# Kernel tuning notes

Hardware: AMD Instinct MI355X
Metric: run time of the kernel (lower is better)

## Reference

```python
import jax, jax.numpy as jnp
import numpy as np

N = 100000   # nodes
R = 4        # relation types
E = 200000   # edges per relation
IN, HID, OUT = 128, 256, 256


def _hetero_conv(x, ew, src, dst, W, b):
    """One HeteroGraphConv(mean) layer of GraphConv(norm='both') per relation.
    x: [N, d_in], ew: [R, E, d_in], src/dst: [R, E], W: [R, d_in, d_out], b: [R, d_out]."""
    outs = []
    for r in range(R):  # small fixed relation set
        s, d = src[r], dst[r]
        ones = jnp.ones((E,), x.dtype)
        deg_out = jax.ops.segment_sum(ones, s, num_segments=N)
        deg_in = jax.ops.segment_sum(ones, d, num_segments=N)
        ns = jax.lax.rsqrt(jnp.clip(deg_out, 1.0))  # src-side norm
        nd = jax.lax.rsqrt(jnp.clip(deg_in, 1.0))   # dst-side norm
        # gather src feats, scale, edge-weight, scatter-sum to dst
        m = x[s] * ns[s][:, None] * ew[r]                       # [E, d_in]
        agg = jax.ops.segment_sum(m, d, num_segments=N)          # [N, d_in]
        agg = agg * nd[:, None]
        outs.append(agg @ W[r] + b[r])
    return sum(outs) / R


def setup_inputs() -> dict:
    key = jax.random.key(0)
    ks = jax.random.split(key, 12)
    sc = 0.05
    return {
        "node_feat": jax.random.normal(ks[0], (N, IN), jnp.float32),
        "edge_w_raw": jax.random.normal(ks[1], (R, E, IN), jnp.float32),
        "src": jax.random.randint(ks[2], (R, E), 0, N),
        "dst": jax.random.randint(ks[3], (R, E), 0, N),
        "Wn": jax.random.normal(ks[4], (IN, HID), jnp.float32) * sc,
        "bn": jax.random.normal(ks[5], (HID,), jnp.float32) * sc,
        "Wr": jax.random.normal(ks[6], (IN, HID), jnp.float32) * sc,
        "br": jax.random.normal(ks[7], (HID,), jnp.float32) * sc,
        "W1": jax.random.normal(ks[8], (R, HID, HID), jnp.float32) * sc,
        "b1": jax.random.normal(ks[9], (R, HID), jnp.float32) * sc,
        "W2": jax.random.normal(ks[10], (R, HID, OUT), jnp.float32) * sc,
        "b2": jax.random.normal(ks[11], (R, OUT), jnp.float32) * sc,
    }


def reference(node_feat, edge_w_raw, src, dst, Wn, bn, Wr, br, W1, b1, W2, b2):
    # rela_fc on raw edge weights (shared by both layers)
    ew = jnp.einsum('rei,ih->reh', edge_w_raw, Wr) + br          # [R, E, HID]
    # node_fc
    x0 = node_feat @ Wn + bn                                      # [N, HID]
    h1 = _hetero_conv(x0, ew, src, dst, W1, b1)                   # [N, HID]
    h2 = _hetero_conv(h1, ew, src, dst, W2, b2)                   # [N, OUT]
    return h2
```

## Files before the change

kernel.cpp:

```cpp
#include <hip/hip_runtime.h>

constexpr int Nn  = 100000;
constexpr int Rr  = 4;
constexpr int Ee  = 200000;
constexpr int Din = 128;
constexpr int Dh  = 256;
constexpr int RN  = Rr * Nn;
constexpr int RE  = Rr * Ee;

typedef float  f32x4  __attribute__((ext_vector_type(4)));
typedef __bf16 bf16x4 __attribute__((ext_vector_type(4)));
typedef __bf16 bf16x8 __attribute__((ext_vector_type(8)));

__global__ __launch_bounds__(256) void count_deg_kernel(
    const int* __restrict__ src, const int* __restrict__ dst,
    int* __restrict__ dego, int* __restrict__ degi) {
  int i = blockIdx.x * 256 + threadIdx.x;
  if (i < RE) {
    int r = i / Ee;
    atomicAdd(&dego[r * Nn + src[i]], 1);
    atomicAdd(&degi[r * Nn + dst[i]], 1);
  }
}

__global__ __launch_bounds__(256) void norms_kernel(
    const int* __restrict__ dego, const int* __restrict__ degi,
    float* __restrict__ ns, float* __restrict__ nd) {
  int i = blockIdx.x * 256 + threadIdx.x;
  if (i < RN) {
    int a = dego[i]; if (a < 1) a = 1;
    int b = degi[i]; if (b < 1) b = 1;
    ns[i] = rsqrtf((float)a);
    nd[i] = rsqrtf((float)b);
  }
}

__device__ inline int block_excl_scan_256(int tsum, int tid, int* wsum) {
  int lane = tid & 63, w = tid >> 6;
  int inc = tsum;
#pragma unroll
  for (int off = 1; off < 64; off <<= 1) {
    int t = __shfl_up(inc, off);
    if (lane >= off) inc += t;
  }
  if (lane == 63) wsum[w] = inc;
  __syncthreads();
  int woff = 0;
  for (int i = 0; i < w; ++i) woff += wsum[i];
  return woff + inc - tsum;
}

__global__ __launch_bounds__(256) void scan1_kernel(
    const int* __restrict__ in, int* __restrict__ out,
    int* __restrict__ partials, int n) {
  __shared__ int wsum[4];
  int tid = threadIdx.x;
  int base = blockIdx.x * 1024 + tid * 4;
  int v[4];
#pragma unroll
  for (int j = 0; j < 4; ++j) v[j] = (base + j < n) ? in[base + j] : 0;
  int tsum = v[0] + v[1] + v[2] + v[3];
  int off = block_excl_scan_256(tsum, tid, wsum);
  int run = off;
#pragma unroll
  for (int j = 0; j < 4; ++j) {
    if (base + j < n) out[base + j] = run;
    run += v[j];
  }
  __syncthreads();
  if (tid == 0) partials[blockIdx.x] = wsum[0] + wsum[1] + wsum[2] + wsum[3];
}

__global__ __launch_bounds__(256) void scan2_kernel(int* __restrict__ p, int n) {
  __shared__ int wsum[4];
  int tid = threadIdx.x;
  int e0 = (2 * tid     < n) ? p[2 * tid]     : 0;
  int e1 = (2 * tid + 1 < n) ? p[2 * tid + 1] : 0;
  int off = block_excl_scan_256(e0 + e1, tid, wsum);
  if (2 * tid     < n) p[2 * tid]     = off;
  if (2 * tid + 1 < n) p[2 * tid + 1] = off + e0;
}

__global__ __launch_bounds__(256) void scan3_kernel(
    int* __restrict__ out, const int* __restrict__ partials, int n) {
  int i = blockIdx.x * 256 + threadIdx.x;
  if (i < n) out[i] += partials[i >> 10];
  if (i == 0) out[n] = RE;
}

__global__ __launch_bounds__(256) void fill_eid_kernel(
    const int* __restrict__ dst, int* __restrict__ cursor,
    int* __restrict__ eid) {
  int i = blockIdx.x * 256 + threadIdx.x;
  if (i < RE) {
    int r = i / Ee;
    int pos = atomicAdd(&cursor[r * Nn + dst[i]], 1);
    eid[pos] = i;
  }
}

__global__ __launch_bounds__(256) void bias_combine_kernel(
    const float* __restrict__ b1, const float* __restrict__ b2,
    float* __restrict__ cb) {
  int i = threadIdx.x;
  cb[i]      = 0.25f * (b1[i] + b1[Dh + i] + b1[2 * Dh + i] + b1[3 * Dh + i]);
  cb[Dh + i] = 0.25f * (b2[i] + b2[Dh + i] + b2[2 * Dh + i] + b2[3 * Dh + i]);
}

__global__ __launch_bounds__(256) void transpose_bf16_kernel(
    const float* __restrict__ in, __bf16* __restrict__ outp, int K) {
  __shared__ float t[32][33];
  int kb = blockIdx.x * 32, nb = blockIdx.y * 32;
  int tx = threadIdx.x & 31, ty = threadIdx.x >> 5;
#pragma unroll
  for (int j = 0; j < 32; j += 8)
    t[ty + j][tx] = in[(size_t)(kb + ty + j) * Dh + nb + tx];
  __syncthreads();
#pragma unroll
  for (int j = 0; j < 32; j += 8)
    outp[(size_t)(nb + ty + j) * K + kb + tx] = (__bf16)t[tx][ty + j];
}

template <int K, bool ABF16, bool OUT_BF16>
__global__ __launch_bounds__(256, 2) void gemm_n256(
    const void* __restrict__ Av, const __bf16* __restrict__ Bt,
    void* __restrict__ Cv, const float* __restrict__ bias,
    float alpha, int M) {
  __shared__ __bf16 As[128][40];
  __shared__ __bf16 Bs[256][40];
  const int tid  = threadIdx.x;
  const int m0   = blockIdx.x * 128;
  const int w    = tid >> 6;
  const int lane = tid & 63;
  const int wr = w >> 1, wc = w & 1;
  const int l15 = lane & 15, quad = lane >> 4;
  f32x4 acc[4][8] = {};

  for (int kt = 0; kt < K / 32; ++kt) {
    if constexpr (ABF16) {
      const __bf16* A = (const __bf16*)Av;
#pragma unroll
      for (int it = 0; it < 2; ++it) {
        int i = tid + it * 256;
        int row = i >> 2;
        int col = (i & 3) << 3;
        int grow = m0 + row;
        bf16x8 v;
#pragma unroll
        for (int j = 0; j < 8; ++j) v[j] = (__bf16)0.f;
        if (grow < M)
          v = *(const bf16x8*)(A + (size_t)grow * K + kt * 32 + col);
        *(bf16x8*)&As[row][col] = v;
      }
    } else {
      const float* A = (const float*)Av;
#pragma unroll
      for (int it = 0; it < 4; ++it) {
        int i = tid + it * 256;
        int row = i >> 3;
        int col = (i & 7) << 2;
        int grow = m0 + row;
        f32x4 v = {0.f, 0.f, 0.f, 0.f};
        if (grow < M)
          v = *(const f32x4*)(A + (size_t)grow * K + kt * 32 + col);
        bf16x4 bv;
        bv[0] = (__bf16)v[0]; bv[1] = (__bf16)v[1];
        bv[2] = (__bf16)v[2]; bv[3] = (__bf16)v[3];
        *(bf16x4*)&As[row][col] = bv;
      }
    }
#pragma unroll
    for (int it = 0; it < 4; ++it) {
      int i = tid + it * 256;
      int n = i >> 2;
      int col = (i & 3) << 3;
      bf16x8 v = *(const bf16x8*)(Bt + (size_t)n * K + kt * 32 + col);
      *(bf16x8*)&Bs[n][col] = v;
    }
    __syncthreads();
    bf16x8 af[4], bfr[8];
#pragma unroll
    for (int mt = 0; mt < 4; ++mt)
      af[mt] = *(const bf16x8*)&As[wr * 64 + mt * 16 + l15][quad * 8];
#pragma unroll
    for (int nt = 0; nt < 8; ++nt)
      bfr[nt] = *(const bf16x8*)&Bs[wc * 128 + nt * 16 + l15][quad * 8];
#pragma unroll
    for (int mt = 0; mt < 4; ++mt)
#pragma unroll
      for (int nt = 0; nt < 8; ++nt)
        acc[mt][nt] = __builtin_amdgcn_mfma_f32_16x16x32_bf16(
            af[mt], bfr[nt], acc[mt][nt], 0, 0, 0);
    __syncthreads();
  }

#pragma unroll
  for (int mt = 0; mt < 4; ++mt) {
    int rl = wr * 64 + mt * 16 + quad * 4;
#pragma unroll
    for (int nt = 0; nt < 8; ++nt) {
      int col = wc * 128 + nt * 16 + l15;
      float bv = bias ? bias[col] : 0.f;
#pragma unroll
      for (int ri = 0; ri < 4; ++ri) {
        int grow = m0 + rl + ri;
        if (grow < M) {
          size_t idx = (size_t)grow * Dh + col;
          float v = alpha * acc[mt][nt][ri] + bv;
          if constexpr (OUT_BF16) {
            ((__bf16*)Cv)[idx] = (__bf16)v;
          } else {
            ((float*)Cv)[idx] = v;
          }
        }
      }
    }
  }
}

__global__ __launch_bounds__(256) void aggregate4_kernel(
    const float* __restrict__ x, const __bf16* __restrict__ ew,
    const int* __restrict__ src, const int* __restrict__ rowptr,
    const int* __restrict__ eid, const float* __restrict__ ns,
    const float* __restrict__ nd, __bf16* __restrict__ agg4) {
  int g = blockIdx.x * 4 + (threadIdx.x >> 6);
  if (g >= RN) return;
  int r = g / Nn;
  int n = g - r * Nn;
  int lane = threadIdx.x & 63;
  int p0 = rowptr[g], p1 = rowptr[g + 1];
  const float* nsr = ns + (size_t)r * Nn;
  f32x4 acc = {0.f, 0.f, 0.f, 0.f};
  for (int p = p0; p < p1; ++p) {
    int ge = eid[p];
    int s = src[ge];
    float sc = nsr[s];
    f32x4  xv = *(const f32x4*)(x + (size_t)s * Dh + lane * 4);
    bf16x4 ev = *(const bf16x4*)(ew + (size_t)ge * Dh + lane * 4);
    acc[0] += xv[0] * sc * (float)ev[0];
    acc[1] += xv[1] * sc * (float)ev[1];
    acc[2] += xv[2] * sc * (float)ev[2];
    acc[3] += xv[3] * sc * (float)ev[3];
  }
  float ndv = nd[g];
  bf16x4 o;
  o[0] = (__bf16)(acc[0] * ndv);
  o[1] = (__bf16)(acc[1] * ndv);
  o[2] = (__bf16)(acc[2] * ndv);
  o[3] = (__bf16)(acc[3] * ndv);
  *(bf16x4*)(agg4 + (size_t)n * (4 * Dh) + (size_t)r * Dh + lane * 4) = o;
}

__global__ __launch_bounds__(256) void edge_scatter_kernel(
    const float* __restrict__ x, const __bf16* __restrict__ ew,
    const int* __restrict__ src, const int* __restrict__ dst,
    const float* __restrict__ ns, const float* __restrict__ nd,
    float* __restrict__ aggf, int cnt) {
  int e = blockIdx.x * 4 + (threadIdx.x >> 6);
  if (e >= cnt) return;
  int lane = threadIdx.x & 63;
  int s = src[e], d = dst[e];
  float sc = ns[s] * nd[d];
  f32x4 xv = *(const f32x4*)(x + (size_t)s * Dh + lane * 4);
  bf16x4 ev = *(const bf16x4*)(ew + (size_t)e * Dh + lane * 4);
  float* ap = aggf + (size_t)d * Dh + lane * 4;
  atomicAdd(ap + 0, xv[0] * sc * (float)ev[0]);
  atomicAdd(ap + 1, xv[1] * sc * (float)ev[1]);
  atomicAdd(ap + 2, xv[2] * sc * (float)ev[2]);
  atomicAdd(ap + 3, xv[3] * sc * (float)ev[3]);
}

__global__ __launch_bounds__(256) void pack_agg_kernel(
    const float* __restrict__ aggf, __bf16* __restrict__ agg4, int r) {
  int i = blockIdx.x * 256 + threadIdx.x;
  if (i < Nn * 64) {
    int n = i >> 6;
    int c = (i & 63) * 4;
    f32x4 v = *(const f32x4*)(aggf + (size_t)n * Dh + c);
    bf16x4 o;
    o[0] = (__bf16)v[0]; o[1] = (__bf16)v[1];
    o[2] = (__bf16)v[2]; o[3] = (__bf16)v[3];
    *(bf16x4*)(agg4 + (size_t)n * (4 * Dh) + (size_t)r * Dh + c) = o;
  }
}

extern "C" void kernel_launch(void* const* d_in, const int* in_sizes, int n_in,
                              void* d_out, int out_size, void* d_ws, size_t ws_size,
                              hipStream_t stream) {
  const float* node_feat  = (const float*)d_in[0];
  const float* edge_w_raw = (const float*)d_in[1];
  const int*   src        = (const int*)d_in[2];
  const int*   dst        = (const int*)d_in[3];
  const float* Wn = (const float*)d_in[4];
  const float* bn = (const float*)d_in[5];
  const float* Wr = (const float*)d_in[6];
  const float* br = (const float*)d_in[7];
  const float* W1 = (const float*)d_in[8];
  const float* b1 = (const float*)d_in[9];
  const float* W2 = (const float*)d_in[10];
  const float* b2 = (const float*)d_in[11];
  float* out = (float*)d_out;

  char* ws = (char*)d_ws;
  size_t off = 0;
  auto alloc = [&](size_t bytes) -> void* {
    void* p = ws + off;
    off += (bytes + 255) & ~(size_t)255;
    return p;
  };
  float*  ns     = (float*)alloc(sizeof(float) * RN);
  float*  nd     = (float*)alloc(sizeof(float) * RN);
  int*    rowptr = (int*)alloc(sizeof(int) * (RN + 1));
  int*    cursor = (int*)alloc(sizeof(int) * RN);
  int*    eid    = (int*)alloc(sizeof(int) * RE);
  int*    parts  = (int*)alloc(sizeof(int) * 512);
  float*  cb     = (float*)alloc(sizeof(float) * 2 * Dh);
  __bf16* BtWn   = (__bf16*)alloc(sizeof(__bf16) * (size_t)Din * Dh);
  __bf16* BtWr   = (__bf16*)alloc(sizeof(__bf16) * (size_t)Din * Dh);
  __bf16* BtW1   = (__bf16*)alloc(sizeof(__bf16) * (size_t)(4 * Dh) * Dh);
  __bf16* BtW2   = (__bf16*)alloc(sizeof(__bf16) * (size_t)(4 * Dh) * Dh);
  float*  x0     = (float*)alloc(sizeof(float) * (size_t)Nn * Dh);
  float*  h1     = (float*)alloc(sizeof(float) * (size_t)Nn * Dh);
  __bf16* agg4   = (__bf16*)alloc(sizeof(__bf16) * (size_t)Nn * 4 * Dh);
  size_t fixed = off;
  size_t ew_full_bytes = (size_t)RE * Dh * 2;
  bool full = (fixed + ew_full_bytes) <= ws_size;
  __bf16* ewb  = nullptr;
  float*  aggf = nullptr;
  int CH = Ee;
  if (full) {
    ewb = (__bf16*)alloc(ew_full_bytes);
  } else {
    aggf = (float*)alloc(sizeof(float) * (size_t)Nn * Dh);
    size_t avail = ws_size > off ? ws_size - off : 0;
    size_t ch = avail / ((size_t)Dh * 2);
    ch = (ch / 512) * 512;
    if (ch > (size_t)Ee) ch = (size_t)Ee;
    if (ch < 512) ch = 512;
    CH = (int)ch;
    ewb = (__bf16*)alloc((size_t)CH * Dh * 2);
  }

  int* dego = (int*)agg4;
  int* degi = dego + RN;
  hipMemsetAsync(dego, 0, sizeof(int) * 2 * (size_t)RN, stream);
  count_deg_kernel<<<(RE + 255) / 256, 256, 0, stream>>>(src, dst, dego, degi);
  norms_kernel<<<(RN + 255) / 256, 256, 0, stream>>>(dego, degi, ns, nd);

  int nchunks = (RN + 1023) / 1024;
  scan1_kernel<<<nchunks, 256, 0, stream>>>(degi, rowptr, parts, RN);
  scan2_kernel<<<1, 256, 0, stream>>>(parts, nchunks);
  scan3_kernel<<<(RN + 255) / 256, 256, 0, stream>>>(rowptr, parts, RN);
  hipMemcpyAsync(cursor, rowptr, sizeof(int) * RN, hipMemcpyDeviceToDevice, stream);
  fill_eid_kernel<<<(RE + 255) / 256, 256, 0, stream>>>(dst, cursor, eid);

  bias_combine_kernel<<<1, 256, 0, stream>>>(b1, b2, cb);
  transpose_bf16_kernel<<<dim3(Din / 32, Dh / 32), 256, 0, stream>>>(Wn, BtWn, Din);
  transpose_bf16_kernel<<<dim3(Din / 32, Dh / 32), 256, 0, stream>>>(Wr, BtWr, Din);
  transpose_bf16_kernel<<<dim3(4 * Dh / 32, Dh / 32), 256, 0, stream>>>(W1, BtW1, 4 * Dh);
  transpose_bf16_kernel<<<dim3(4 * Dh / 32, Dh / 32), 256, 0, stream>>>(W2, BtW2, 4 * Dh);

  gemm_n256<Din, false, false><<<(Nn + 127) / 128, 256, 0, stream>>>(
      node_feat, BtWn, x0, bn, 1.0f, Nn);

  if (full) {
    gemm_n256<Din, false, true><<<RE / 128, 256, 0, stream>>>(
        edge_w_raw, BtWr, ewb, br, 1.0f, RE);
  }

  for (int layer = 0; layer < 2; ++layer) {
    const float*  x   = layer ? h1 : x0;
    float*        o   = layer ? out : h1;
    const __bf16* Bt  = layer ? BtW2 : BtW1;
    const float*  cbl = cb + layer * Dh;
    if (full) {
      aggregate4_kernel<<<(RN + 3) / 4, 256, 0, stream>>>(
          x, ewb, src, rowptr, eid, ns, nd, agg4);
    } else {
      for (int r = 0; r < Rr; ++r) {
        hipMemsetAsync(aggf, 0, sizeof(float) * (size_t)Nn * Dh, stream);
        for (int c0 = 0; c0 < Ee; c0 += CH) {
          int cnt = (Ee - c0 < CH) ? (Ee - c0) : CH;
          gemm_n256<Din, false, true><<<(cnt + 127) / 128, 256, 0, stream>>>(
              edge_w_raw + ((size_t)r * Ee + c0) * Din, BtWr, ewb, br, 1.0f, cnt);
          edge_scatter_kernel<<<(cnt + 3) / 4, 256, 0, stream>>>(
              x, ewb, src + (size_t)r * Ee + c0, dst + (size_t)r * Ee + c0,
              ns + (size_t)r * Nn, nd + (size_t)r * Nn, aggf, cnt);
        }
        pack_agg_kernel<<<(Nn * 64 + 255) / 256, 256, 0, stream>>>(aggf, agg4, r);
      }
    }
    gemm_n256<4 * Dh, true, false><<<(Nn + 127) / 128, 256, 0, stream>>>(
        agg4, Bt, o, cbl, 0.25f, Nn);
  }
}
```

Before: 1.959 ms.

## Replace LDS-tiled GEMM with register-direct streaming GEMM and unroll aggregation by two

Measured after the change: 2.146 ms. +9.5%, slower.

```diff
diff --git a/kernel.cpp b/kernel.cpp
--- a/kernel.cpp
+++ b/kernel.cpp
@@ -122,88 +122,74 @@
 }
 
 template <int K, bool ABF16, bool OUT_BF16>
-__global__ __launch_bounds__(256, 2) void gemm_n256(
+__global__ __launch_bounds__(256) void gemm_stream(
     const void* __restrict__ Av, const __bf16* __restrict__ Bt,
     void* __restrict__ Cv, const float* __restrict__ bias,
     float alpha, int M) {
-  __shared__ __bf16 As[128][40];
-  __shared__ __bf16 Bs[256][40];
   const int tid  = threadIdx.x;
-  const int m0   = blockIdx.x * 128;
   const int w    = tid >> 6;
   const int lane = tid & 63;
-  const int wr = w >> 1, wc = w & 1;
-  const int l15 = lane & 15, quad = lane >> 4;
-  f32x4 acc[4][8] = {};
-
+  const int l15  = lane & 15, quad = lane >> 4;
+  const int m0   = blockIdx.x * 64;
+  const int n0   = w * 64;
+
+  f32x4 acc[4][4] = {};
+
+  int arow[4];
+#pragma unroll
+  for (int mt = 0; mt < 4; ++mt) {
+    int r = m0 + mt * 16 + l15;
+    arow[mt] = (r < M) ? r : (M - 1);
+  }
+
+#pragma unroll 4
   for (int kt = 0; kt < K / 32; ++kt) {
+    const int kk = kt * 32 + quad * 8;
+    bf16x8 bfrag[4];
+#pragma unroll
+    for (int nt = 0; nt < 4; ++nt) {
+      int n = n0 + nt * 16 + l15;
+      bfrag[nt] = *(const bf16x8*)(Bt + (size_t)n * K + kk);
+    }
+    bf16x8 afrag[4];
     if constexpr (ABF16) {
       const __bf16* A = (const __bf16*)Av;
 #pragma unroll
-      for (int it = 0; it < 2; ++it) {
-        int i = tid + it * 256;
-        int row = i >> 2;
-        int col = (i & 3) << 3;
-        int grow = m0 + row;
-        bf16x8 v;
-#pragma unroll
-        for (int j = 0; j < 8; ++j) v[j] = (__bf16)0.f;
-        if (grow < M)
-          v = *(const bf16x8*)(A + (size_t)grow * K + kt * 32 + col);
-        *(bf16x8*)&As[row][col] = v;
-      }
+      for (int mt = 0; mt < 4; ++mt)
+        afrag[mt] = *(const bf16x8*)(A + (size_t)arow[mt] * K + kk);
     } else {
       const float* A = (const float*)Av;
 #pragma unroll
-      for (int it = 0; it < 4; ++it) {
-        int i = tid + it * 256;
-        int row = i >> 3;
-        int col = (i & 7) << 2;
-        int grow = m0 + row;
-        f32x4 v = {0.f, 0.f, 0.f, 0.f};
-        if (grow < M)
-          v = *(const f32x4*)(A + (size_t)grow * K + kt * 32 + col);
-        bf16x4 bv;
-        bv[0] = (__bf16)v[0]; bv[1] = (__bf16)v[1];
-        bv[2] = (__bf16)v[2]; bv[3] = (__bf16)v[3];
-        *(bf16x4*)&As[row][col] = bv;
+      for (int mt = 0; mt < 4; ++mt) {
+        const float* ap = A + (size_t)arow[mt] * K + kk;
+        f32x4 v0 = *(const f32x4*)(ap);
+        f32x4 v1 = *(const f32x4*)(ap + 4);
+        bf16x8 t;
+        t[0] = (__bf16)v0[0]; t[1] = (__bf16)v0[1];
+        t[2] = (__bf16)v0[2]; t[3] = (__bf16)v0[3];
+        t[4] = (__bf16)v1[0]; t[5] = (__bf16)v1[1];
+        t[6] = (__bf16)v1[2]; t[7] = (__bf16)v1[3];
+        afrag[mt] = t;
       }
     }
 #pragma unroll
-    for (int it = 0; it < 4; ++it) {
-      int i = tid + it * 256;
-      int n = i >> 2;
-      int col = (i & 3) << 3;
-      bf16x8 v = *(const bf16x8*)(Bt + (size_t)n * K + kt * 32 + col);
-      *(bf16x8*)&Bs[n][col] = v;
-    }
-    __syncthreads();
-    bf16x8 af[4], bfr[8];
-#pragma unroll
     for (int mt = 0; mt < 4; ++mt)
-      af[mt] = *(const bf16x8*)&As[wr * 64 + mt * 16 + l15][quad * 8];
-#pragma unroll
-    for (int nt = 0; nt < 8; ++nt)
-      bfr[nt] = *(const bf16x8*)&Bs[wc * 128 + nt * 16 + l15][quad * 8];
-#pragma unroll
-    for (int mt = 0; mt < 4; ++mt)
-#pragma unroll
-      for (int nt = 0; nt < 8; ++nt)
+#pragma unroll
+      for (int nt = 0; nt < 4; ++nt)
         acc[mt][nt] = __builtin_amdgcn_mfma_f32_16x16x32_bf16(
-            af[mt], bfr[nt], acc[mt][nt], 0, 0, 0);
-    __syncthreads();
+            afrag[mt], bfrag[nt], acc[mt][nt], 0, 0, 0);
   }
 
 #pragma unroll
   for (int mt = 0; mt < 4; ++mt) {
-    int rl = wr * 64 + mt * 16 + quad * 4;
-#pragma unroll
-    for (int nt = 0; nt < 8; ++nt) {
-      int col = wc * 128 + nt * 16 + l15;
+    int rl = m0 + mt * 16 + quad * 4;
+#pragma unroll
+    for (int nt = 0; nt < 4; ++nt) {
+      int col = n0 + nt * 16 + l15;
       float bv = bias ? bias[col] : 0.f;
 #pragma unroll
       for (int ri = 0; ri < 4; ++ri) {
-        int grow = m0 + rl + ri;
+        int grow = rl + ri;
         if (grow < M) {
           size_t idx = (size_t)grow * Dh + col;
           float v = alpha * acc[mt][nt][ri] + bv;
@@ -231,16 +217,22 @@
   int p0 = rowptr[g], p1 = rowptr[g + 1];
   const float* nsr = ns + (size_t)r * Nn;
   f32x4 acc = {0.f, 0.f, 0.f, 0.f};
-  for (int p = p0; p < p1; ++p) {
-    int ge = eid[p];
-    int s = src[ge];
-    float sc = nsr[s];
-    f32x4  xv = *(const f32x4*)(x + (size_t)s * Dh + lane * 4);
-    bf16x4 ev = *(const bf16x4*)(ew + (size_t)ge * Dh + lane * 4);
-    acc[0] += xv[0] * sc * (float)ev[0];
-    acc[1] += xv[1] * sc * (float)ev[1];
-    acc[2] += xv[2] * sc * (float)ev[2];
-    acc[3] += xv[3] * sc * (float)ev[3];
+  for (int p = p0; p < p1; p += 2) {
+    int  geA  = eid[p];
+    bool hasB = (p + 1 < p1);
+    int  geB  = hasB ? eid[p + 1] : geA;
+    int sA = src[geA];
+    int sB = src[geB];
+    float scA = nsr[sA];
+    float scB = hasB ? nsr[sB] : 0.f;
+    f32x4  xA = *(const f32x4*)(x + (size_t)sA * Dh + lane * 4);
+    bf16x4 eA = *(const bf16x4*)(ew + (size_t)geA * Dh + lane * 4);
+    f32x4  xB = *(const f32x4*)(x + (size_t)sB * Dh + lane * 4);
+    bf16x4 eB = *(const bf16x4*)(ew + (size_t)geB * Dh + lane * 4);
+    acc[0] += xA[0] * scA * (float)eA[0] + xB[0] * scB * (float)eB[0];
+    acc[1] += xA[1] * scA * (float)eA[1] + xB[1] * scB * (float)eB[1];
+    acc[2] += xA[2] * scA * (float)eA[2] + xB[2] * scB * (float)eB[2];
+    acc[3] += xA[3] * scA * (float)eA[3] + xB[3] * scB * (float)eB[3];
   }
   float ndv = nd[g];
   bf16x4 o;
@@ -360,11 +352,11 @@
   transpose_bf16_kernel<<<dim3(4 * Dh / 32, Dh / 32), 256, 0, stream>>>(W1, BtW1, 4 * Dh);
   transpose_bf16_kernel<<<dim3(4 * Dh / 32, Dh / 32), 256, 0, stream>>>(W2, BtW2, 4 * Dh);
 
-  gemm_n256<Din, false, false><<<(Nn + 127) / 128, 256, 0, stream>>>(
+  gemm_stream<Din, false, false><<<(Nn + 63) / 64, 256, 0, stream>>>(
       node_feat, BtWn, x0, bn, 1.0f, Nn);
 
   if (full) {
-    gemm_n256<Din, false, true><<<RE / 128, 256, 0, stream>>>(
+    gemm_stream<Din, false, true><<<RE / 64, 256, 0, stream>>>(
         edge_w_raw, BtWr, ewb, br, 1.0f, RE);
   }
 
@@ -381,7 +373,7 @@
         hipMemsetAsync(aggf, 0, sizeof(float) * (size_t)Nn * Dh, stream);
         for (int c0 = 0; c0 < Ee; c0 += CH) {
           int cnt = (Ee - c0 < CH) ? (Ee - c0) : CH;
-          gemm_n256<Din, false, true><<<(cnt + 127) / 128, 256, 0, stream>>>(
+          gemm_stream<Din, false, true><<<(cnt + 63) / 64, 256, 0, stream>>>(
               edge_w_raw + ((size_t)r * Ee + c0) * Din, BtWr, ewb, br, 1.0f, cnt);
           edge_scatter_kernel<<<(cnt + 3) / 4, 256, 0, stream>>>(
               x, ewb, src + (size_t)r * Ee + c0, dst + (size_t)r * Ee + c0,
@@ -390,7 +382,7 @@
         pack_agg_kernel<<<(Nn * 64 + 255) / 256, 256, 0, stream>>>(aggf, agg4, r);
       }
     }
-    gemm_n256<4 * Dh, true, false><<<(Nn + 127) / 128, 256, 0, stream>>>(
+    gemm_stream<4 * Dh, true, false><<<(Nn + 63) / 64, 256, 0, stream>>>(
         agg4, Bt, o, cbl, 0.25f, Nn);
   }
 }
```
